# Kernel tuning notes

Hardware: AMD Instinct MI355X
Metric: run time of the kernel (lower is better)

## Reference

```python
import jax, jax.numpy as jnp
import numpy as np

BETA = 0.95      # snn.Leaky(beta=0.95)
THRESHOLD = 1.0  # snntorch default
STEPS = 10


def setup_inputs() -> dict:
    key = jax.random.key(0)
    k1, k2 = jax.random.split(key)
    x = jax.random.normal(k1, (65536, 784), dtype=jnp.float32)
    # fc weight [out=10, in=784], no bias
    W = jax.random.normal(k2, (10, 784), dtype=jnp.float32) * (1.0 / np.sqrt(784.0))
    return {"x": x, "W": W}


def reference(x, W):
    # x: [B, 784] (already flat); fc(x) is the same every step -> compute once.
    cur = x @ W.T  # [B, 10]
    # snntorch Leaky (reset-by-subtraction):
    #   reset_t = spk_{t-1}; mem_t = beta*mem_{t-1} + cur - reset_t*thr; spk_t = (mem_t > thr)
    def step(carry, _):
        mem, spk = carry
        mem = BETA * mem + cur - spk * THRESHOLD
        spk = (mem > THRESHOLD).astype(cur.dtype)
        return (mem, spk), spk

    init = (jnp.zeros_like(cur), jnp.zeros_like(cur))
    _, spk_rec = jax.lax.scan(step, init, None, length=STEPS)  # [STEPS, B, 10]
    return spk_rec.sum(axis=0)  # [B, 10]
```

## Files before the change

kernel.cpp:

```cpp
#include <hip/hip_runtime.h>


constexpr int ROWS = 65536;
constexpr int COLS = 784;
constexpr int NOUT = 10;
constexpr int STEPS = 10;

constexpr int BR   = 64;
constexpr int TW   = 16;
constexpr int NT   = COLS / TW;
constexpr int PADW = TW + 1;
constexpr int NH   = 8;
constexpr int CPH  = TW / NH;

__global__ void w_to_f64(const float* __restrict__ W, double* __restrict__ W64) {
    int i = blockIdx.x * 256 + threadIdx.x;
    if (i < NOUT * COLS) W64[i] = (double)W[i];
}

__global__ __launch_bounds__(512, 8)
void snn_fused(const float* __restrict__ x, const double* __restrict__ W64,
               float* __restrict__ out) {
    __shared__ __align__(16) char smem[NH * BR * NOUT * 8];
    float*  tile = reinterpret_cast<float*>(smem);
    double* comb = reinterpret_cast<double*>(smem);

    const int tid  = threadIdx.x;
    const int r    = tid & (BR - 1);
    const int h    = tid >> 6;
    const int hu   = __builtin_amdgcn_readfirstlane(h);
    const int row0 = blockIdx.x * BR;

    const float* xblk = x + (size_t)row0 * COLS;

    float4 cv;
    auto issue = [&](int t, float4& v) {
        if (tid < BR * TW / 4) {
            int rr = tid >> 2, c4 = tid & 3;
            v = *reinterpret_cast<const float4*>(xblk + (size_t)rr * COLS + t * TW + c4 * 4);
        }
    };
    auto wlds = [&](int b, const float4& v) {
        if (tid < BR * TW / 4) {
            int rr = tid >> 2, c4 = tid & 3;
            float* p = tile + b * (BR * PADW) + rr * PADW + c4 * 4;
            p[0] = v.x; p[1] = v.y; p[2] = v.z; p[3] = v.w;
        }
    };

    double acc[NOUT];
    #pragma unroll
    for (int j = 0; j < NOUT; ++j) acc[j] = 0.0;

    issue(0, cv);
    wlds(0, cv);
    __syncthreads();

    for (int t = 0; t < NT; ++t) {
        float4 nv;
        if (t + 1 < NT) issue(t + 1, nv);

        const float*  src = tile + (t & 1) * (BR * PADW) + r * PADW + hu * CPH;
        const double* wb  = W64 + t * TW + hu * CPH;
        #pragma unroll
        for (int c = 0; c < CPH; ++c) {
            double xd = (double)src[c];
            #pragma unroll
            for (int j = 0; j < NOUT; ++j)
                acc[j] = fma(xd, wb[j * COLS + c], acc[j]);
        }

        if (t + 1 < NT) wlds((t + 1) & 1, nv);
        __syncthreads();
    }

    #pragma unroll
    for (int j = 0; j < NOUT; ++j)
        comb[hu * (BR * NOUT) + r * NOUT + j] = acc[j];
    __syncthreads();

    for (int i = tid; i < BR * NOUT; i += 512) {
        double cur = 0.0;
        #pragma unroll
        for (int hh = 0; hh < NH; ++hh)
            cur += comb[hh * (BR * NOUT) + i];

        double mem = 0.0, spk = 0.0, s = 0.0;
        #pragma unroll
        for (int st = 0; st < STEPS; ++st) {
            mem = 0.95 * mem + cur - spk;
            spk = (mem > 1.0) ? 1.0 : 0.0;
            s  += spk;
        }
        out[(size_t)row0 * NOUT + i] = (float)s;
    }
}

extern "C" void kernel_launch(void* const* d_in, const int* in_sizes, int n_in,
                              void* d_out, int out_size, void* d_ws, size_t ws_size,
                              hipStream_t stream) {
    const float* x = (const float*)d_in[0];
    const float* W = (const float*)d_in[1];
    float*  out = (float*)d_out;
    double* W64 = (double*)d_ws;

    hipLaunchKernelGGL(w_to_f64, dim3((NOUT * COLS + 255) / 256), dim3(256), 0, stream, W, W64);
    hipLaunchKernelGGL(snn_fused, dim3(ROWS / BR), dim3(512), 0, stream, x, W64, out);
}
```

Before: 48.46 us.

## Stream x rows directly from global into registers, dropping LDS tiling

Each thread now reads its own row's column quarter straight from global memory with float4 loads and register double-buffering, instead of staging 64x16 tiles through shared memory with a barrier every tile. W is transposed in the prep kernel so each column's 10 weights sit together, and the block shrinks to 256 threads with four column quarters reduced through LDS. This removes per-tile syncthreads and LDS traffic. The cost is that lanes read rows 3 KB apart, so each wave load is uncoalesced across lanes and depends on cache-line reuse over iterations.

```diff
diff --git a/kernel.cpp b/kernel.cpp
--- a/kernel.cpp
+++ b/kernel.cpp
@@ -1,89 +1,66 @@
 #include <hip/hip_runtime.h>
 
 
-constexpr int ROWS = 65536;
-constexpr int COLS = 784;
-constexpr int NOUT = 10;
+constexpr int ROWS  = 65536;
+constexpr int COLS  = 784;
+constexpr int NOUT  = 10;
 constexpr int STEPS = 10;
 
-constexpr int BR   = 64;
-constexpr int TW   = 16;
-constexpr int NT   = COLS / TW;
-constexpr int PADW = TW + 1;
-constexpr int NH   = 8;
-constexpr int CPH  = TW / NH;
+constexpr int QN  = 4;
+constexpr int QC  = COLS / QN;
+constexpr int NIT = QC / 4;
+constexpr int BRW = 64;
 
-__global__ void w_to_f64(const float* __restrict__ W, double* __restrict__ W64) {
+__global__ void w_prep(const float* __restrict__ W, double* __restrict__ W64T) {
     int i = blockIdx.x * 256 + threadIdx.x;
-    if (i < NOUT * COLS) W64[i] = (double)W[i];
+    if (i < NOUT * COLS) {
+        int c = i / NOUT, j = i - c * NOUT;
+        W64T[i] = (double)W[(size_t)j * COLS + c];
+    }
 }
 
-__global__ __launch_bounds__(512, 8)
-void snn_fused(const float* __restrict__ x, const double* __restrict__ W64,
-               float* __restrict__ out) {
-    __shared__ __align__(16) char smem[NH * BR * NOUT * 8];
-    float*  tile = reinterpret_cast<float*>(smem);
-    double* comb = reinterpret_cast<double*>(smem);
+__global__ __launch_bounds__(256, 4)
+void snn_stream(const float* __restrict__ x, const double* __restrict__ W64T,
+                float* __restrict__ out) {
+    __shared__ double part[QN * BRW * NOUT];
 
-    const int tid  = threadIdx.x;
-    const int r    = tid & (BR - 1);
-    const int h    = tid >> 6;
-    const int hu   = __builtin_amdgcn_readfirstlane(h);
-    const int row0 = blockIdx.x * BR;
+    const int tid = threadIdx.x;
+    const int l   = tid & 63;
+    const int q   = __builtin_amdgcn_readfirstlane(tid >> 6);
+    const size_t row0 = (size_t)blockIdx.x * BRW;
 
-    const float* xblk = x + (size_t)row0 * COLS;
-
-    float4 cv;
-    auto issue = [&](int t, float4& v) {
-        if (tid < BR * TW / 4) {
-            int rr = tid >> 2, c4 = tid & 3;
-            v = *reinterpret_cast<const float4*>(xblk + (size_t)rr * COLS + t * TW + c4 * 4);
-        }
-    };
-    auto wlds = [&](int b, const float4& v) {
-        if (tid < BR * TW / 4) {
-            int rr = tid >> 2, c4 = tid & 3;
-            float* p = tile + b * (BR * PADW) + rr * PADW + c4 * 4;
-            p[0] = v.x; p[1] = v.y; p[2] = v.z; p[3] = v.w;
-        }
-    };
+    const float*  xp = x + (row0 + l) * COLS + q * QC;
+    const double* wp = W64T + q * QC * NOUT;
 
     double acc[NOUT];
     #pragma unroll
     for (int j = 0; j < NOUT; ++j) acc[j] = 0.0;
 
-    issue(0, cv);
-    wlds(0, cv);
-    __syncthreads();
-
-    for (int t = 0; t < NT; ++t) {
-        float4 nv;
-        if (t + 1 < NT) issue(t + 1, nv);
-
-        const float*  src = tile + (t & 1) * (BR * PADW) + r * PADW + hu * CPH;
-        const double* wb  = W64 + t * TW + hu * CPH;
+    float4 cur = *reinterpret_cast<const float4*>(xp);
+    #pragma unroll 7
+    for (int it = 0; it < NIT; ++it) {
+        int itn = (it + 1 < NIT) ? it + 1 : NIT - 1;
+        float4 nxt = *reinterpret_cast<const float4*>(xp + itn * 4);
+        const double* wb = wp + it * 4 * NOUT;
         #pragma unroll
-        for (int c = 0; c < CPH; ++c) {
-            double xd = (double)src[c];
+        for (int c = 0; c < 4; ++c) {
+            double xd = (double)((&cur.x)[c]);
             #pragma unroll
             for (int j = 0; j < NOUT; ++j)
-                acc[j] = fma(xd, wb[j * COLS + c], acc[j]);
+                acc[j] = fma(xd, wb[c * NOUT + j], acc[j]);
         }
-
-        if (t + 1 < NT) wlds((t + 1) & 1, nv);
-        __syncthreads();
+        cur = nxt;
     }
 
     #pragma unroll
     for (int j = 0; j < NOUT; ++j)
-        comb[hu * (BR * NOUT) + r * NOUT + j] = acc[j];
+        part[(q * BRW + l) * NOUT + j] = acc[j];
     __syncthreads();
 
-    for (int i = tid; i < BR * NOUT; i += 512) {
-        double cur = 0.0;
-        #pragma unroll
-        for (int hh = 0; hh < NH; ++hh)
-            cur += comb[hh * (BR * NOUT) + i];
+    for (int i = tid; i < BRW * NOUT; i += 256) {
+        double c0  = part[i]                 + part[BRW * NOUT + i];
+        double c1  = part[2 * BRW * NOUT + i] + part[3 * BRW * NOUT + i];
+        double cur = c0 + c1;
 
         double mem = 0.0, spk = 0.0, s = 0.0;
         #pragma unroll
@@ -92,7 +69,7 @@
             spk = (mem > 1.0) ? 1.0 : 0.0;
             s  += spk;
         }
-        out[(size_t)row0 * NOUT + i] = (float)s;
+        out[row0 * NOUT + i] = (float)s;
     }
 }
 
@@ -101,9 +78,9 @@
                               hipStream_t stream) {
     const float* x = (const float*)d_in[0];
     const float* W = (const float*)d_in[1];
-    float*  out = (float*)d_out;
-    double* W64 = (double*)d_ws;
+    float*  out  = (float*)d_out;
+    double* W64T = (double*)d_ws;
 
-    hipLaunchKernelGGL(w_to_f64, dim3((NOUT * COLS + 255) / 256), dim3(256), 0, stream, W, W64);
-    hipLaunchKernelGGL(snn_fused, dim3(ROWS / BR), dim3(512), 0, stream, x, W64, out);
+    hipLaunchKernelGGL(w_prep, dim3((NOUT * COLS + 255) / 256), dim3(256), 0, stream, W, W64T);
+    hipLaunchKernelGGL(snn_stream, dim3(ROWS / BRW), dim3(256), 0, stream, x, W64T, out);
 }
```

Measured after the change: 68.40 us. 1.41x slower.

## Widen K-tile to 56 columns and transpose FP64 weights for contiguous loads

Applied to the files above, without the earlier changes.

Raises the per-iteration column tile from 16 to 56, so the loop runs 14 times instead of 49. That means fewer barriers, and all 512 threads help stage x, with two float4 loads each. The weight prep kernel now stores W transposed as [col][out] in double, so each thread reads its 10 outputs contiguously and the scalar loads can merge. The head reduction becomes a pairwise tree. The shared-memory tile still fits inside the existing buffer (2*64*57 floats is under 40960 bytes), but the larger live register set may reduce occupancy.

```diff
diff --git a/kernel.cpp b/kernel.cpp
--- a/kernel.cpp
+++ b/kernel.cpp
@@ -1,25 +1,29 @@
 #include <hip/hip_runtime.h>
 
 
-constexpr int ROWS = 65536;
-constexpr int COLS = 784;
-constexpr int NOUT = 10;
+constexpr int ROWS  = 65536;
+constexpr int COLS  = 784;
+constexpr int NOUT  = 10;
 constexpr int STEPS = 10;
 
 constexpr int BR   = 64;
-constexpr int TW   = 16;
+constexpr int TW   = 56;
 constexpr int NT   = COLS / TW;
 constexpr int PADW = TW + 1;
 constexpr int NH   = 8;
 constexpr int CPH  = TW / NH;
+constexpr int NF4  = BR * TW / 4;
 
-__global__ void w_to_f64(const float* __restrict__ W, double* __restrict__ W64) {
+__global__ void w_prep(const float* __restrict__ W, double* __restrict__ W64T) {
     int i = blockIdx.x * 256 + threadIdx.x;
-    if (i < NOUT * COLS) W64[i] = (double)W[i];
+    if (i < NOUT * COLS) {
+        int c = i / NOUT, j = i - c * NOUT;
+        W64T[i] = (double)W[(size_t)j * COLS + c];
+    }
 }
 
 __global__ __launch_bounds__(512, 8)
-void snn_fused(const float* __restrict__ x, const double* __restrict__ W64,
+void snn_fused(const float* __restrict__ x, const double* __restrict__ W64T,
                float* __restrict__ out) {
     __shared__ __align__(16) char smem[NH * BR * NOUT * 8];
     float*  tile = reinterpret_cast<float*>(smem);
@@ -27,24 +31,33 @@
 
     const int tid  = threadIdx.x;
     const int r    = tid & (BR - 1);
-    const int h    = tid >> 6;
-    const int hu   = __builtin_amdgcn_readfirstlane(h);
-    const int row0 = blockIdx.x * BR;
+    const int hu   = __builtin_amdgcn_readfirstlane(tid >> 6);
+    const size_t row0 = (size_t)blockIdx.x * BR;
 
-    const float* xblk = x + (size_t)row0 * COLS;
+    const float* xblk = x + row0 * COLS;
 
-    float4 cv;
-    auto issue = [&](int t, float4& v) {
-        if (tid < BR * TW / 4) {
-            int rr = tid >> 2, c4 = tid & 3;
-            v = *reinterpret_cast<const float4*>(xblk + (size_t)rr * COLS + t * TW + c4 * 4);
+    float4 cv[2];
+    auto issue = [&](int t, float4* v) {
+        const float* xb = xblk + t * TW;
+        #pragma unroll
+        for (int k = 0; k < 2; ++k) {
+            int i = tid + 512 * k;
+            if (i < NF4) {
+                int rr = i / (TW / 4), c4 = i % (TW / 4);
+                v[k] = *reinterpret_cast<const float4*>(xb + (size_t)rr * COLS + c4 * 4);
+            }
         }
     };
-    auto wlds = [&](int b, const float4& v) {
-        if (tid < BR * TW / 4) {
-            int rr = tid >> 2, c4 = tid & 3;
-            float* p = tile + b * (BR * PADW) + rr * PADW + c4 * 4;
-            p[0] = v.x; p[1] = v.y; p[2] = v.z; p[3] = v.w;
+    auto wlds = [&](int b, const float4* v) {
+        float* dst = tile + b * (BR * PADW);
+        #pragma unroll
+        for (int k = 0; k < 2; ++k) {
+            int i = tid + 512 * k;
+            if (i < NF4) {
+                int rr = i / (TW / 4), c4 = i % (TW / 4);
+                float* p = dst + rr * PADW + c4 * 4;
+                p[0] = v[k].x; p[1] = v[k].y; p[2] = v[k].z; p[3] = v[k].w;
+            }
         }
     };
 
@@ -57,17 +70,17 @@
     __syncthreads();
 
     for (int t = 0; t < NT; ++t) {
-        float4 nv;
+        float4 nv[2];
         if (t + 1 < NT) issue(t + 1, nv);
 
         const float*  src = tile + (t & 1) * (BR * PADW) + r * PADW + hu * CPH;
-        const double* wb  = W64 + t * TW + hu * CPH;
+        const double* wb  = W64T + (size_t)(t * TW + hu * CPH) * NOUT;
         #pragma unroll
         for (int c = 0; c < CPH; ++c) {
             double xd = (double)src[c];
             #pragma unroll
             for (int j = 0; j < NOUT; ++j)
-                acc[j] = fma(xd, wb[j * COLS + c], acc[j]);
+                acc[j] = fma(xd, wb[c * NOUT + j], acc[j]);
         }
 
         if (t + 1 < NT) wlds((t + 1) & 1, nv);
@@ -76,14 +89,15 @@
 
     #pragma unroll
     for (int j = 0; j < NOUT; ++j)
-        comb[hu * (BR * NOUT) + r * NOUT + j] = acc[j];
+        comb[(hu * BR + r) * NOUT + j] = acc[j];
     __syncthreads();
 
     for (int i = tid; i < BR * NOUT; i += 512) {
-        double cur = 0.0;
-        #pragma unroll
-        for (int hh = 0; hh < NH; ++hh)
-            cur += comb[hh * (BR * NOUT) + i];
+        double c0 = comb[i]                  + comb[BR * NOUT + i];
+        double c1 = comb[2 * BR * NOUT + i]  + comb[3 * BR * NOUT + i];
+        double c2 = comb[4 * BR * NOUT + i]  + comb[5 * BR * NOUT + i];
+        double c3 = comb[6 * BR * NOUT + i]  + comb[7 * BR * NOUT + i];
+        double cur = (c0 + c1) + (c2 + c3);
 
         double mem = 0.0, spk = 0.0, s = 0.0;
         #pragma unroll
@@ -92,7 +106,7 @@
             spk = (mem > 1.0) ? 1.0 : 0.0;
             s  += spk;
         }
-        out[(size_t)row0 * NOUT + i] = (float)s;
+        out[row0 * NOUT + i] = (float)s;
     }
 }
 
@@ -101,9 +115,9 @@
                               hipStream_t stream) {
     const float* x = (const float*)d_in[0];
     const float* W = (const float*)d_in[1];
-    float*  out = (float*)d_out;
-    double* W64 = (double*)d_ws;
+    float*  out  = (float*)d_out;
+    double* W64T = (double*)d_ws;
 
-    hipLaunchKernelGGL(w_to_f64, dim3((NOUT * COLS + 255) / 256), dim3(256), 0, stream, W, W64);
-    hipLaunchKernelGGL(snn_fused, dim3(ROWS / BR), dim3(512), 0, stream, x, W64, out);
+    hipLaunchKernelGGL(w_prep, dim3((NOUT * COLS + 255) / 256), dim3(256), 0, stream, W, W64T);
+    hipLaunchKernelGGL(snn_fused, dim3(ROWS / BR), dim3(512), 0, stream, x, W64T, out);
 }
```

After: 81.11 us. +67.4%, slower.
